# Kernel optimization log

Measured on AMD Instinct MI355X. Metric: run time of the kernel, lower is better.

Reference implementation:

```python
import jax, jax.numpy as jnp
import numpy as np

H_IMG = 224
W_IMG = 224
CHUNK = 128   # triangles rasterized per scan step
EPS = 1e-8
N_VERTS = 6890
N_FACES = 13776
BATCH = 2


def setup_inputs() -> dict:
    key = jax.random.key(0)
    k0, k1, k2 = jax.random.split(key, 3)
    # vertices in front of the camera (z ~ 2.5) so triangles project into the image
    v = jax.random.normal(k0, (BATCH, N_VERTS, 3), jnp.float32) * 0.3 + jnp.array([0.0, 0.0, 2.5], jnp.float32)
    vc = jax.random.uniform(k1, (N_VERTS, 3), dtype=jnp.float32)          # per-vertex colors
    f = jax.random.randint(k2, (N_FACES, 3), 0, N_VERTS, dtype=jnp.int32)  # triangle list
    bgcolor = jnp.zeros((3,), jnp.float32)
    camera_f = jnp.array([500.0, 500.0], jnp.float32)
    camera_c = jnp.array([112.0, 112.0], jnp.float32)
    camera_t = jnp.zeros((3,), jnp.float32)
    camera_rt = jnp.zeros((3,), jnp.float32)
    return {"v": v, "vc": vc, "bgcolor": bgcolor, "camera_f": camera_f,
            "camera_c": camera_c, "camera_t": camera_t, "camera_rt": camera_rt, "f": f}


def _rodrigues(r):
    # axis-angle -> rotation matrix, safe at r = 0
    th = jnp.sqrt(jnp.sum(r * r) + 1e-12)
    k = r / th
    kx, ky, kz = k[0], k[1], k[2]
    z = jnp.zeros_like(kx)
    K = jnp.stack([jnp.stack([z, -kz, ky]),
                   jnp.stack([kz, z, -kx]),
                   jnp.stack([-ky, kx, z])])
    c, s = jnp.cos(th), jnp.sin(th)
    return c * jnp.eye(3, dtype=r.dtype) + (1.0 - c) * jnp.outer(k, k) + s * K


def _edge(ax, ay, bx, by, px, py):
    # signed area of (a, b, p) * 2
    return (bx - ax) * (py - ay) - (by - ay) * (px - ax)


def _rasterize(uv, zc, vc, faces, bgcolor, height, width):
    """Z-buffered rasterization with perspective-correct barycentric color interp.
    uv: [V,2] screen coords, zc: [V] camera-space depth, vc: [V,C], faces: [F,3]."""
    F, C = faces.shape[0], vc.shape[-1]
    pad = (-F) % CHUNK
    faces_p = jnp.concatenate([faces, jnp.zeros((pad, 3), faces.dtype)], 0)
    fmask = jnp.concatenate([jnp.ones((F,), bool), jnp.zeros((pad,), bool)])
    faces_p = faces_p.reshape(-1, CHUNK, 3)
    fmask = fmask.reshape(-1, CHUNK)

    xs = jnp.arange(width, dtype=jnp.float32) + 0.5
    ys = jnp.arange(height, dtype=jnp.float32) + 0.5
    px, py = jnp.meshgrid(xs, ys)              # [H,W] pixel centers
    cx = px.ravel()[None, :]                    # [1,HW]
    cy = py.ravel()[None, :]
    HW = height * width
    ar = jnp.arange(HW)

    def step(carry, inp):
        zbuf, col = carry
        fc, fm = inp                            # [K,3] int, [K] bool
        p = uv[fc]                              # [K,3,2]
        zt = zc[fc]                             # [K,3]
        x0, y0 = p[:, 0, 0:1], p[:, 0, 1:2]
        x1, y1 = p[:, 1, 0:1], p[:, 1, 1:2]
        x2, y2 = p[:, 2, 0:1], p[:, 2, 1:2]
        w0 = _edge(x1, y1, x2, y2, cx, cy)      # [K,HW]
        w1 = _edge(x2, y2, x0, y0, cx, cy)
        w2 = _edge(x0, y0, x1, y1, cx, cy)
        area = _edge(x0, y0, x1, y1, x2, y2)    # [K,1]
        nz = jnp.abs(area) > EPS
        inv_area = jnp.where(nz, 1.0 / jnp.where(nz, area, 1.0), 0.0)
        b0, b1, b2 = w0 * inv_area, w1 * inv_area, w2 * inv_area
        inside = (b0 >= 0) & (b1 >= 0) & (b2 >= 0)
        zvalid = jnp.all(zt > EPS, axis=1, keepdims=True)
        valid = inside & zvalid & nz & fm[:, None]
        zt_s = jnp.maximum(zt, EPS)
        inv_z = b0 / zt_s[:, 0:1] + b1 / zt_s[:, 1:2] + b2 / zt_s[:, 2:3]
        zp = jnp.where(valid & (inv_z > EPS), 1.0 / jnp.maximum(inv_z, EPS), jnp.inf)
        idx = jnp.argmin(zp, axis=0)            # nearest triangle per pixel in chunk
        zmin = zp[idx, ar]                      # [HW]
        hit = jnp.isfinite(zmin)
        zmin_s = jnp.where(hit, zmin, 1.0)
        bb = jnp.stack([b0, b1, b2], -1)[idx, ar]   # [HW,3]
        fsel = fc[idx]                          # [HW,3]
        zsel = jnp.maximum(zt[idx], EPS)        # [HW,3]
        csel = vc[fsel]                         # [HW,3,C]
        pc = bb / zsel                          # perspective-correct weights / z
        newcol = jnp.einsum('pk,pkc->pc', pc, csel) * zmin_s[:, None]
        upd = hit & (zmin < zbuf)
        zbuf = jnp.where(upd, zmin_s, zbuf)
        col = jnp.where(upd[:, None], newcol, col)
        return (zbuf, col), None

    zbuf0 = jnp.full((HW,), jnp.inf, jnp.float32)
    col0 = jnp.broadcast_to(bgcolor.astype(jnp.float32), (HW, C))
    (zbuf, col), _ = jax.lax.scan(step, (zbuf0, col0), (faces_p, fmask))
    return col.reshape(height, width, C)


def reference(v, vc, bgcolor, camera_f, camera_c, camera_t, camera_rt, f):
    R = _rodrigues(camera_rt)
    vcam = jnp.einsum('bvj,ij->bvi', v, R) + camera_t   # [B,V,3]
    z = vcam[..., 2]
    zs = jnp.maximum(z, EPS)
    uv = vcam[..., :2] / zs[..., None] * camera_f + camera_c  # pinhole projection
    render = jax.vmap(lambda uv_b, z_b: _rasterize(uv_b, z_b, vc, f, bgcolor, H_IMG, W_IMG))
    return render(uv, z)                                   # [B,H,W,C]
```

## Files before the change

kernel.cpp:

```cpp
#include <hip/hip_runtime.h>
#include <math.h>

#define H_IMG 224
#define W_IMG 224
#define HW (H_IMG * W_IMG)
#define EPSF 1e-8f
#define NV 6890
#define NF 13776
#define NB 2
#define FCHUNK 128
#define NCHUNK ((NF + FCHUNK - 1) / FCHUNK)
#define FPAD (NCHUNK * FCHUNK)
#define NBUCK 1024
#define CHDR_STRIDE 128
#define KEY_INIT 0x7F800000FFFFFFFFULL

#define OFF_VERTS 0u
#define OFF_ZBU   220672u
#define OFF_ZBS   331008u
#define OFF_BBS   441600u
#define OFF_GMS   883968u
#define OFF_OIS   2653440u
#define OFF_INV   2764032u
#define OFF_CHDR  2874368u
#define OFF_CNT   2875392u
#define OFF_OFFS  2883584u

__device__ inline unsigned long long shfl_xor_u64(unsigned long long v, int m) {
  unsigned lo = (unsigned)v, hi = (unsigned)(v >> 32);
  lo = __shfl_xor(lo, m);
  hi = __shfl_xor(hi, m);
  return ((unsigned long long)hi << 32) | lo;
}

__global__ void proj_init_kernel(const float* __restrict__ v,
                                 const float* __restrict__ cf,
                                 const float* __restrict__ cc,
                                 const float* __restrict__ ct,
                                 const float* __restrict__ crt,
                                 float4* __restrict__ verts,
                                 float* __restrict__ zbS, float4* __restrict__ bbS,
                                 unsigned* __restrict__ chdr, unsigned* __restrict__ cnt) {
  int i = blockIdx.x * blockDim.x + threadIdx.x;
  if (i < NB * NV) {
    float r0 = crt[0], r1 = crt[1], r2 = crt[2];
    float ss = __fadd_rn(__fadd_rn(__fmul_rn(r0, r0), __fmul_rn(r1, r1)), __fmul_rn(r2, r2));
    float th = sqrtf(__fadd_rn(ss, 1e-12f));
    float kx = r0 / th, ky = r1 / th, kz = r2 / th;
    float c = cosf(th), s = sinf(th), oc = 1.0f - c;
    float R00 = c + oc * kx * kx,      R01 = oc * kx * ky - s * kz, R02 = oc * kx * kz + s * ky;
    float R10 = oc * ky * kx + s * kz, R11 = c + oc * ky * ky,      R12 = oc * ky * kz - s * kx;
    float R20 = oc * kz * kx - s * ky, R21 = oc * kz * ky + s * kx, R22 = c + oc * kz * kz;
    float x = v[i * 3 + 0], y = v[i * 3 + 1], z = v[i * 3 + 2];
    float xc = R00 * x + R01 * y + R02 * z + ct[0];
    float yc = R10 * x + R11 * y + R12 * z + ct[1];
    float zc = R20 * x + R21 * y + R22 * z + ct[2];
    float zs = fmaxf(zc, EPSF);
    float u = __fadd_rn(__fmul_rn(xc / zs, cf[0]), cc[0]);
    float w = __fadd_rn(__fmul_rn(yc / zs, cf[1]), cc[1]);
    verts[i] = make_float4(u, w, zc, 0.0f);
  }
  if (i < NB * FPAD) {
    zbS[i] = 3e30f;
    bbS[i] = make_float4(1e30f, -1e30f, 1e30f, -1e30f);
  }
  if (i < NB * CHDR_STRIDE) chdr[i] = 0x7F800000u;
  if (i < NB * NBUCK) cnt[i] = 0u;
}

__global__ void zb_kernel(const int* __restrict__ f, const float4* __restrict__ verts,
                          float* __restrict__ zbU, unsigned* __restrict__ cnt) {
  int i = blockIdx.x * blockDim.x + threadIdx.x;
  if (i >= NB * NF) return;
  int b = i / NF, fi = i - b * NF;
  int i0 = f[fi * 3 + 0], i1 = f[fi * 3 + 1], i2 = f[fi * 3 + 2];
  float4 p0 = verts[b * NV + i0], p1 = verts[b * NV + i1], p2 = verts[b * NV + i2];
  float area = __fsub_rn(__fmul_rn(__fsub_rn(p1.x, p0.x), __fsub_rn(p2.y, p0.y)),
                         __fmul_rn(__fsub_rn(p1.y, p0.y), __fsub_rn(p2.x, p0.x)));
  bool nz = fabsf(area) > EPSF;
  bool zv = (p0.z > EPSF) && (p1.z > EPSF) && (p2.z > EPSF);
  bool ok = nz && zv;
  float zb;
  if (!ok) {
    zb = 3e30f;
  } else {
    float minz = fminf(fminf(fmaxf(p0.z, EPSF), fmaxf(p1.z, EPSF)), fmaxf(p2.z, EPSF));
    float M = fmaxf(fmaxf(fmaxf(fabsf(p0.x), fabsf(p0.y)), fmaxf(fabsf(p1.x), fabsf(p1.y))),
                    fmaxf(fabsf(p2.x), fabsf(p2.y)));
    float werr = (2.0f * M) * (M + 256.0f) * 6e-7f;
    bool tight = (3.0f * werr) <= (5e-4f * fabsf(area));
    zb = tight ? __fmul_rn(minz, 0.999f) : 0.0f;
  }
  zbU[i] = zb;
  int bucket = (int)fminf(fmaxf(zb * 256.0f, 0.0f), (float)(NBUCK - 1));
  atomicAdd(&cnt[b * NBUCK + bucket], 1u);
}

__global__ __launch_bounds__(1024) void scan_kernel(const unsigned* __restrict__ cnt,
                                                    unsigned* __restrict__ offs) {
  __shared__ unsigned wsum[16];
  int t = threadIdx.x, b = blockIdx.x;
  int lane = t & 63, wid = t >> 6;
  unsigned v = cnt[b * NBUCK + t];
  unsigned acc = v;
  #pragma unroll
  for (int d = 1; d < 64; d <<= 1) {
    unsigned n = __shfl_up(acc, d);
    if (lane >= d) acc += n;
  }
  if (lane == 63) wsum[wid] = acc;
  __syncthreads();
  if (t < 16) {
    unsigned wv = wsum[t];
    #pragma unroll
    for (int d = 1; d < 16; d <<= 1) {
      unsigned n = __shfl_up(wv, d, 16);
      if (t >= d) wv += n;
    }
    wsum[t] = wv;
  }
  __syncthreads();
  unsigned base = (wid > 0) ? wsum[wid - 1] : 0u;
  offs[b * NBUCK + t] = base + acc - v;
}

__global__ void scatter_kernel(const int* __restrict__ f, const float4* __restrict__ verts,
                               const float* __restrict__ zbU, unsigned* __restrict__ offs,
                               float* __restrict__ zbS, float4* __restrict__ bbS,
                               float4* __restrict__ gmS, int* __restrict__ oiS,
                               int* __restrict__ inv, unsigned* __restrict__ chdr) {
  int i = blockIdx.x * blockDim.x + threadIdx.x;
  if (i >= NB * NF) return;
  int b = i / NF, fi = i - b * NF;
  float zb = zbU[i];
  int bucket = (int)fminf(fmaxf(zb * 256.0f, 0.0f), (float)(NBUCK - 1));
  unsigned pos = atomicAdd(&offs[b * NBUCK + bucket], 1u);
  int i0 = f[fi * 3 + 0], i1 = f[fi * 3 + 1], i2 = f[fi * 3 + 2];
  float4 p0 = verts[b * NV + i0], p1 = verts[b * NV + i1], p2 = verts[b * NV + i2];
  float x0 = p0.x, y0 = p0.y, z0 = p0.z;
  float x1 = p1.x, y1 = p1.y, z1 = p1.z;
  float x2 = p2.x, y2 = p2.y, z2 = p2.z;
  float area = __fsub_rn(__fmul_rn(__fsub_rn(x1, x0), __fsub_rn(y2, y0)),
                         __fmul_rn(__fsub_rn(y1, y0), __fsub_rn(x2, x0)));
  bool nz = fabsf(area) > EPSF;
  float inv_area = nz ? (1.0f / area) : 0.0f;
  bool zv = (z0 > EPSF) && (z1 > EPSF) && (z2 > EPSF);
  bool ok = nz && zv;
  float zz0 = ok ? fmaxf(z0, EPSF) : 1e30f;
  float zz1 = ok ? fmaxf(z1, EPSF) : 1e30f;
  float zz2 = ok ? fmaxf(z2, EPSF) : 1e30f;
  size_t sp_ = (size_t)b * FPAD + pos;
  zbS[sp_] = zb;
  bbS[sp_] = make_float4(fminf(fminf(x0, x1), x2), fmaxf(fmaxf(x0, x1), x2),
                         fminf(fminf(y0, y1), y2), fmaxf(fmaxf(y0, y1), y2));
  gmS[sp_ * 4 + 0] = make_float4(__fsub_rn(x2, x1), __fsub_rn(y2, y1), x1, y1);
  gmS[sp_ * 4 + 1] = make_float4(__fsub_rn(x0, x2), __fsub_rn(y0, y2), x2, y2);
  gmS[sp_ * 4 + 2] = make_float4(__fsub_rn(x1, x0), __fsub_rn(y1, y0), x0, y0);
  gmS[sp_ * 4 + 3] = make_float4(zz0, zz1, zz2, inv_area);
  oiS[sp_] = fi;
  inv[i] = (int)pos;
  atomicMin(&chdr[b * CHDR_STRIDE + (int)(pos / FCHUNK)], __float_as_uint(zb));
}

__global__ __launch_bounds__(CHDR_STRIDE) void suffix_kernel(unsigned* __restrict__ chdr) {
  __shared__ unsigned s[CHDR_STRIDE];
  int t = threadIdx.x, b = blockIdx.x;
  s[t] = chdr[b * CHDR_STRIDE + t];
  __syncthreads();
  for (int d = 1; d < CHDR_STRIDE; d <<= 1) {
    unsigned v = (t + d < CHDR_STRIDE) ? s[t + d] : 0x7F800000u;
    __syncthreads();
    s[t] = (v < s[t]) ? v : s[t];
    __syncthreads();
  }
  chdr[b * CHDR_STRIDE + t] = s[t];
}

__global__ __launch_bounds__(256) void raster_kernel(
    const unsigned* __restrict__ chdr,
    const float* __restrict__ zbS,
    const float4* __restrict__ bbS,
    const float4* __restrict__ gmS,
    const int* __restrict__ oiS,
    const int* __restrict__ inv,
    const int* __restrict__ f,
    const float* __restrict__ vc,
    const float* __restrict__ bg,
    float* __restrict__ out) {
  __shared__ unsigned hint[4][16];
  __shared__ unsigned long long fin[4][16];
  int b = blockIdx.z;
  int w = threadIdx.x >> 6;
  int lane = threadIdx.x & 63;
  int slot = lane & 3;
  int p = lane >> 2;
  int wx = blockIdx.x * 4, wy = blockIdx.y * 4;
  int x = wx + (p & 3), y = wy + (p >> 2);
  float px = (float)x + 0.5f, py = (float)y + 0.5f;
  float tx0 = (float)wx + 0.5f, tx1 = (float)wx + 3.5f;
  float ty0 = (float)wy + 0.5f, ty1 = (float)wy + 3.5f;
  const unsigned* chdrB = chdr + b * CHDR_STRIDE;
  const float*  zbB = zbS + (size_t)b * FPAD;
  const float4* bbB = bbS + (size_t)b * FPAD;
  const float4* gmB = gmS + (size_t)b * FPAD * 4;
  const int*    oiB = oiS + (size_t)b * FPAD;

  if (threadIdx.x < 64) hint[threadIdx.x >> 4][threadIdx.x & 15] = 0x7F800000u;
  __syncthreads();

  unsigned long long bestKey = KEY_INIT;

  for (int c = w; c < NCHUNK; c += 4) {
    unsigned z_ = (unsigned)(bestKey >> 32);
    unsigned zo = __shfl_xor(z_, 1); if (zo < z_) z_ = zo;
    zo = __shfl_xor(z_, 2); if (zo < z_) z_ = zo;
    if (slot == 0) hint[w][p] = z_;
    unsigned bzp = hint[0][p];
    unsigned h1 = hint[1][p]; if (h1 < bzp) bzp = h1;
    unsigned h2 = hint[2][p]; if (h2 < bzp) bzp = h2;
    unsigned h3 = hint[3][p]; if (h3 < bzp) bzp = h3;
    float comb = __uint_as_float(bzp);
    float czb = __uint_as_float(chdrB[c]);
    if (!__any(czb <= comb)) break;
    float combMax = fmaxf(comb, __shfl_xor(comb, 4));
    combMax = fmaxf(combMax, __shfl_xor(combMax, 8));
    combMax = fmaxf(combMax, __shfl_xor(combMax, 16));
    combMax = fmaxf(combMax, __shfl_xor(combMax, 32));
    int base = c * FCHUNK;
    #pragma unroll
    for (int h = 0; h < FCHUNK / 64; ++h) {
      int fbase = base + h * 64;
      float zb_lane = zbB[fbase + lane];
      float4 bb = bbB[fbase + lane];
      bool pass = (zb_lane <= combMax) &&
                  (bb.x <= tx1) && (bb.y >= tx0) &&
                  (bb.z <= ty1) && (bb.w >= ty0);
      unsigned long long m = __ballot(pass);
      unsigned long long mm = m;
      while (mm) {
        int bit = __builtin_ctzll(mm);
        int g = bit & ~3;
        mm &= ~(0xFULL << g);
        if ((m >> (g + slot)) & 1) {
          int fi = fbase + g + slot;
          const float4* gm = &gmB[(size_t)fi * 4];
          float4 q0 = gm[0], q1 = gm[1], q2 = gm[2], q3 = gm[3];
          float w0 = __fsub_rn(__fmul_rn(q0.x, __fsub_rn(py, q0.w)),
                               __fmul_rn(q0.y, __fsub_rn(px, q0.z)));
          float w1 = __fsub_rn(__fmul_rn(q1.x, __fsub_rn(py, q1.w)),
                               __fmul_rn(q1.y, __fsub_rn(px, q1.z)));
          float w2 = __fsub_rn(__fmul_rn(q2.x, __fsub_rn(py, q2.w)),
                               __fmul_rn(q2.y, __fsub_rn(px, q2.z)));
          float b0 = __fmul_rn(w0, q3.w);
          float b1 = __fmul_rn(w1, q3.w);
          float b2 = __fmul_rn(w2, q3.w);
          if (b0 >= 0.0f && b1 >= 0.0f && b2 >= 0.0f) {
            float invz = __fadd_rn(__fadd_rn(b0 / q3.x, b1 / q3.y), b2 / q3.z);
            if (invz > EPSF) {
              float zp = 1.0f / invz;
              unsigned long long key =
                  ((unsigned long long)__float_as_uint(zp) << 32) | (unsigned)oiB[fi];
              if (key < bestKey) bestKey = key;
            }
          }
        }
      }
    }
  }

  unsigned long long o = shfl_xor_u64(bestKey, 1);
  if (o < bestKey) bestKey = o;
  o = shfl_xor_u64(bestKey, 2);
  if (o < bestKey) bestKey = o;
  if (slot == 0) fin[w][p] = bestKey;
  __syncthreads();

  int t = threadIdx.x;
  if (t < 16) {
    unsigned long long key = fin[0][t];
    unsigned long long k1 = fin[1][t]; if (k1 < key) key = k1;
    unsigned long long k2 = fin[2][t]; if (k2 < key) key = k2;
    unsigned long long k3 = fin[3][t]; if (k3 < key) key = k3;
    int xx = wx + (t & 3), yy = wy + (t >> 2);
    float pxx = (float)xx + 0.5f, pyy = (float)yy + 0.5f;
    float o0, o1, o2;
    if (key != KEY_INIT) {
      int best = (int)(unsigned)(key & 0xFFFFFFFFu);
      float zmin = __uint_as_float((unsigned)(key >> 32));
      int pos = inv[b * NF + best];
      const float4* g = &gmB[(size_t)pos * 4];
      float4 q0 = g[0], q1 = g[1], q2 = g[2], q3 = g[3];
      float w0 = __fsub_rn(__fmul_rn(q0.x, __fsub_rn(pyy, q0.w)),
                           __fmul_rn(q0.y, __fsub_rn(pxx, q0.z)));
      float w1 = __fsub_rn(__fmul_rn(q1.x, __fsub_rn(pyy, q1.w)),
                           __fmul_rn(q1.y, __fsub_rn(pxx, q1.z)));
      float w2 = __fsub_rn(__fmul_rn(q2.x, __fsub_rn(pyy, q2.w)),
                           __fmul_rn(q2.y, __fsub_rn(pxx, q2.z)));
      float b0 = __fmul_rn(w0, q3.w), b1 = __fmul_rn(w1, q3.w), b2 = __fmul_rn(w2, q3.w);
      float pc0 = b0 / q3.x, pc1 = b1 / q3.y, pc2 = b2 / q3.z;
      int i0 = f[best * 3 + 0], i1 = f[best * 3 + 1], i2 = f[best * 3 + 2];
      const float* c0p = vc + (size_t)i0 * 3;
      const float* c1p = vc + (size_t)i1 * 3;
      const float* c2p = vc + (size_t)i2 * 3;
      o0 = __fmul_rn(__fadd_rn(__fadd_rn(__fmul_rn(pc0, c0p[0]), __fmul_rn(pc1, c1p[0])),
                               __fmul_rn(pc2, c2p[0])), zmin);
      o1 = __fmul_rn(__fadd_rn(__fadd_rn(__fmul_rn(pc0, c0p[1]), __fmul_rn(pc1, c1p[1])),
                               __fmul_rn(pc2, c2p[1])), zmin);
      o2 = __fmul_rn(__fadd_rn(__fadd_rn(__fmul_rn(pc0, c0p[2]), __fmul_rn(pc1, c1p[2])),
                               __fmul_rn(pc2, c2p[2])), zmin);
    } else {
      o0 = bg[0]; o1 = bg[1]; o2 = bg[2];
    }
    size_t oo = ((size_t)(b * H_IMG + yy) * W_IMG + xx) * 3;
    out[oo + 0] = o0;
    out[oo + 1] = o1;
    out[oo + 2] = o2;
  }
}

extern "C" void kernel_launch(void* const* d_in, const int* in_sizes, int n_in,
                              void* d_out, int out_size, void* d_ws, size_t ws_size,
                              hipStream_t stream) {
  const float* v   = (const float*)d_in[0];
  const float* vc  = (const float*)d_in[1];
  const float* bg  = (const float*)d_in[2];
  const float* cf  = (const float*)d_in[3];
  const float* cc  = (const float*)d_in[4];
  const float* ct  = (const float*)d_in[5];
  const float* crt = (const float*)d_in[6];
  const int*   f   = (const int*)d_in[7];
  float* out = (float*)d_out;
  char* ws = (char*)d_ws;

  float4*   verts = (float4*)(ws + OFF_VERTS);
  float*    zbU   = (float*)(ws + OFF_ZBU);
  float*    zbS   = (float*)(ws + OFF_ZBS);
  float4*   bbS   = (float4*)(ws + OFF_BBS);
  float4*   gmS   = (float4*)(ws + OFF_GMS);
  int*      oiS   = (int*)(ws + OFF_OIS);
  int*      inv   = (int*)(ws + OFF_INV);
  unsigned* chdr  = (unsigned*)(ws + OFF_CHDR);
  unsigned* cnt   = (unsigned*)(ws + OFF_CNT);
  unsigned* offs  = (unsigned*)(ws + OFF_OFFS);

  hipLaunchKernelGGL(proj_init_kernel, dim3((NB * HW + 255) / 256), dim3(256), 0, stream,
                     v, cf, cc, ct, crt, verts, zbS, bbS, chdr, cnt);
  hipLaunchKernelGGL(zb_kernel, dim3((NB * NF + 255) / 256), dim3(256), 0, stream,
                     f, verts, zbU, cnt);
  hipLaunchKernelGGL(scan_kernel, dim3(NB), dim3(1024), 0, stream, cnt, offs);
  hipLaunchKernelGGL(scatter_kernel, dim3((NB * NF + 255) / 256), dim3(256), 0, stream,
                     f, verts, zbU, offs, zbS, bbS, gmS, oiS, inv, chdr);
  hipLaunchKernelGGL(suffix_kernel, dim3(NB), dim3(CHDR_STRIDE), 0, stream, chdr);
  hipLaunchKernelGGL(raster_kernel, dim3(W_IMG / 4, H_IMG / 4, NB),
                     dim3(256), 0, stream,
                     chdr, zbS, bbS, gmS, oiS, inv, f, vc, bg, out);
}
```

Baseline: 302.1 us.

## Fuse projection into face kernels, derive chunk bounds in scan, use 8 waves

Removes the separate vertex-projection kernel: each face kernel now recomputes the camera transform and projects its three vertices inline. The per-chunk minimum-depth header is computed in the scan kernel by binary search over bucket ends, which drops the atomicMin in scatter and the suffix kernel. The count reset moves to a memset, and the raster kernel grows from 4 to 8 waves per tile to split the chunk loop further. This trades fewer launches and atomics for redundant projection math, a coarser bucket-level depth bound, and more waves contending on the shared hint.

```diff
diff --git a/kernel.cpp b/kernel.cpp
--- a/kernel.cpp
+++ b/kernel.cpp
@@ -11,20 +11,20 @@
 #define FCHUNK 128
 #define NCHUNK ((NF + FCHUNK - 1) / FCHUNK)
 #define FPAD (NCHUNK * FCHUNK)
+#define NWAVE 8
 #define NBUCK 1024
 #define CHDR_STRIDE 128
 #define KEY_INIT 0x7F800000FFFFFFFFULL
 
-#define OFF_VERTS 0u
-#define OFF_ZBU   220672u
-#define OFF_ZBS   331008u
-#define OFF_BBS   441600u
-#define OFF_GMS   883968u
-#define OFF_OIS   2653440u
-#define OFF_INV   2764032u
-#define OFF_CHDR  2874368u
-#define OFF_CNT   2875392u
-#define OFF_OFFS  2883584u
+#define OFF_ZBU   0u
+#define OFF_ZBS   110336u
+#define OFF_BBS   220928u
+#define OFF_GMS   663296u
+#define OFF_OIS   2432768u
+#define OFF_INV   2543360u
+#define OFF_CHDR  2653696u
+#define OFF_CNT   2654720u
+#define OFF_OFFS  2662912u
 
 __device__ inline unsigned long long shfl_xor_u64(unsigned long long v, int m) {
   unsigned lo = (unsigned)v, hi = (unsigned)(v >> 32);
@@ -33,48 +33,52 @@
   return ((unsigned long long)hi << 32) | lo;
 }
 
-__global__ void proj_init_kernel(const float* __restrict__ v,
-                                 const float* __restrict__ cf,
-                                 const float* __restrict__ cc,
-                                 const float* __restrict__ ct,
-                                 const float* __restrict__ crt,
-                                 float4* __restrict__ verts,
-                                 float* __restrict__ zbS, float4* __restrict__ bbS,
-                                 unsigned* __restrict__ chdr, unsigned* __restrict__ cnt) {
+struct Cam { float m[9]; float t0, t1, t2, fx, fy, cx, cy; };
+
+__device__ inline Cam load_cam(const float* cf, const float* cc,
+                               const float* ct, const float* crt) {
+  Cam C;
+  float r0 = crt[0], r1 = crt[1], r2 = crt[2];
+  float ss = __fadd_rn(__fadd_rn(__fmul_rn(r0, r0), __fmul_rn(r1, r1)), __fmul_rn(r2, r2));
+  float th = sqrtf(__fadd_rn(ss, 1e-12f));
+  float kx = r0 / th, ky = r1 / th, kz = r2 / th;
+  float c = cosf(th), s = sinf(th), oc = 1.0f - c;
+  C.m[0] = c + oc * kx * kx;      C.m[1] = oc * kx * ky - s * kz; C.m[2] = oc * kx * kz + s * ky;
+  C.m[3] = oc * ky * kx + s * kz; C.m[4] = c + oc * ky * ky;      C.m[5] = oc * ky * kz - s * kx;
+  C.m[6] = oc * kz * kx - s * ky; C.m[7] = oc * kz * ky + s * kx; C.m[8] = c + oc * kz * kz;
+  C.t0 = ct[0]; C.t1 = ct[1]; C.t2 = ct[2];
+  C.fx = cf[0]; C.fy = cf[1]; C.cx = cc[0]; C.cy = cc[1];
+  return C;
+}
+
+__device__ inline float3 proj_one(const Cam& C, const float* vp) {
+  float x = vp[0], y = vp[1], z = vp[2];
+  float xc = C.m[0] * x + C.m[1] * y + C.m[2] * z + C.t0;
+  float yc = C.m[3] * x + C.m[4] * y + C.m[5] * z + C.t1;
+  float zc = C.m[6] * x + C.m[7] * y + C.m[8] * z + C.t2;
+  float zs = fmaxf(zc, EPSF);
+  float u = __fadd_rn(__fmul_rn(xc / zs, C.fx), C.cx);
+  float w = __fadd_rn(__fmul_rn(yc / zs, C.fy), C.cy);
+  return make_float3(u, w, zc);
+}
+
+__global__ void zb_init_kernel(const float* __restrict__ v, const int* __restrict__ f,
+                               const float* __restrict__ cf, const float* __restrict__ cc,
+                               const float* __restrict__ ct, const float* __restrict__ crt,
+                               float* __restrict__ zbU, unsigned* __restrict__ cnt,
+                               float* __restrict__ zbS, float4* __restrict__ bbS) {
   int i = blockIdx.x * blockDim.x + threadIdx.x;
-  if (i < NB * NV) {
-    float r0 = crt[0], r1 = crt[1], r2 = crt[2];
-    float ss = __fadd_rn(__fadd_rn(__fmul_rn(r0, r0), __fmul_rn(r1, r1)), __fmul_rn(r2, r2));
-    float th = sqrtf(__fadd_rn(ss, 1e-12f));
-    float kx = r0 / th, ky = r1 / th, kz = r2 / th;
-    float c = cosf(th), s = sinf(th), oc = 1.0f - c;
-    float R00 = c + oc * kx * kx,      R01 = oc * kx * ky - s * kz, R02 = oc * kx * kz + s * ky;
-    float R10 = oc * ky * kx + s * kz, R11 = c + oc * ky * ky,      R12 = oc * ky * kz - s * kx;
-    float R20 = oc * kz * kx - s * ky, R21 = oc * kz * ky + s * kx, R22 = c + oc * kz * kz;
-    float x = v[i * 3 + 0], y = v[i * 3 + 1], z = v[i * 3 + 2];
-    float xc = R00 * x + R01 * y + R02 * z + ct[0];
-    float yc = R10 * x + R11 * y + R12 * z + ct[1];
-    float zc = R20 * x + R21 * y + R22 * z + ct[2];
-    float zs = fmaxf(zc, EPSF);
-    float u = __fadd_rn(__fmul_rn(xc / zs, cf[0]), cc[0]);
-    float w = __fadd_rn(__fmul_rn(yc / zs, cf[1]), cc[1]);
-    verts[i] = make_float4(u, w, zc, 0.0f);
-  }
   if (i < NB * FPAD) {
     zbS[i] = 3e30f;
     bbS[i] = make_float4(1e30f, -1e30f, 1e30f, -1e30f);
   }
-  if (i < NB * CHDR_STRIDE) chdr[i] = 0x7F800000u;
-  if (i < NB * NBUCK) cnt[i] = 0u;
-}
-
-__global__ void zb_kernel(const int* __restrict__ f, const float4* __restrict__ verts,
-                          float* __restrict__ zbU, unsigned* __restrict__ cnt) {
-  int i = blockIdx.x * blockDim.x + threadIdx.x;
   if (i >= NB * NF) return;
   int b = i / NF, fi = i - b * NF;
+  Cam C = load_cam(cf, cc, ct, crt);
   int i0 = f[fi * 3 + 0], i1 = f[fi * 3 + 1], i2 = f[fi * 3 + 2];
-  float4 p0 = verts[b * NV + i0], p1 = verts[b * NV + i1], p2 = verts[b * NV + i2];
+  float3 p0 = proj_one(C, v + ((size_t)b * NV + i0) * 3);
+  float3 p1 = proj_one(C, v + ((size_t)b * NV + i1) * 3);
+  float3 p2 = proj_one(C, v + ((size_t)b * NV + i2) * 3);
   float area = __fsub_rn(__fmul_rn(__fsub_rn(p1.x, p0.x), __fsub_rn(p2.y, p0.y)),
                          __fmul_rn(__fsub_rn(p1.y, p0.y), __fsub_rn(p2.x, p0.x)));
   bool nz = fabsf(area) > EPSF;
@@ -97,8 +101,10 @@
 }
 
 __global__ __launch_bounds__(1024) void scan_kernel(const unsigned* __restrict__ cnt,
-                                                    unsigned* __restrict__ offs) {
+                                                    unsigned* __restrict__ offs,
+                                                    unsigned* __restrict__ chdr) {
   __shared__ unsigned wsum[16];
+  __shared__ unsigned ends[NBUCK];
   int t = threadIdx.x, b = blockIdx.x;
   int lane = t & 63, wid = t >> 6;
   unsigned v = cnt[b * NBUCK + t];
@@ -121,22 +127,39 @@
   }
   __syncthreads();
   unsigned base = (wid > 0) ? wsum[wid - 1] : 0u;
-  offs[b * NBUCK + t] = base + acc - v;
-}
-
-__global__ void scatter_kernel(const int* __restrict__ f, const float4* __restrict__ verts,
+  unsigned incl = base + acc;
+  offs[b * NBUCK + t] = incl - v;
+  ends[t] = incl;
+  __syncthreads();
+  if (t < NCHUNK) {
+    unsigned pos0 = (unsigned)(t * FCHUNK);
+    int lo = 0, hi = NBUCK - 1;
+    while (lo < hi) {
+      int mid = (lo + hi) >> 1;
+      if (ends[mid] > pos0) hi = mid; else lo = mid + 1;
+    }
+    chdr[b * CHDR_STRIDE + t] = __float_as_uint((float)lo * (1.0f / 256.0f));
+  }
+}
+
+__global__ void scatter_kernel(const float* __restrict__ v, const int* __restrict__ f,
+                               const float* __restrict__ cf, const float* __restrict__ cc,
+                               const float* __restrict__ ct, const float* __restrict__ crt,
                                const float* __restrict__ zbU, unsigned* __restrict__ offs,
                                float* __restrict__ zbS, float4* __restrict__ bbS,
                                float4* __restrict__ gmS, int* __restrict__ oiS,
-                               int* __restrict__ inv, unsigned* __restrict__ chdr) {
+                               int* __restrict__ inv) {
   int i = blockIdx.x * blockDim.x + threadIdx.x;
   if (i >= NB * NF) return;
   int b = i / NF, fi = i - b * NF;
   float zb = zbU[i];
   int bucket = (int)fminf(fmaxf(zb * 256.0f, 0.0f), (float)(NBUCK - 1));
   unsigned pos = atomicAdd(&offs[b * NBUCK + bucket], 1u);
+  Cam C = load_cam(cf, cc, ct, crt);
   int i0 = f[fi * 3 + 0], i1 = f[fi * 3 + 1], i2 = f[fi * 3 + 2];
-  float4 p0 = verts[b * NV + i0], p1 = verts[b * NV + i1], p2 = verts[b * NV + i2];
+  float3 p0 = proj_one(C, v + ((size_t)b * NV + i0) * 3);
+  float3 p1 = proj_one(C, v + ((size_t)b * NV + i1) * 3);
+  float3 p2 = proj_one(C, v + ((size_t)b * NV + i2) * 3);
   float x0 = p0.x, y0 = p0.y, z0 = p0.z;
   float x1 = p1.x, y1 = p1.y, z1 = p1.z;
   float x2 = p2.x, y2 = p2.y, z2 = p2.z;
@@ -159,24 +182,9 @@
   gmS[sp_ * 4 + 3] = make_float4(zz0, zz1, zz2, inv_area);
   oiS[sp_] = fi;
   inv[i] = (int)pos;
-  atomicMin(&chdr[b * CHDR_STRIDE + (int)(pos / FCHUNK)], __float_as_uint(zb));
-}
-
-__global__ __launch_bounds__(CHDR_STRIDE) void suffix_kernel(unsigned* __restrict__ chdr) {
-  __shared__ unsigned s[CHDR_STRIDE];
-  int t = threadIdx.x, b = blockIdx.x;
-  s[t] = chdr[b * CHDR_STRIDE + t];
-  __syncthreads();
-  for (int d = 1; d < CHDR_STRIDE; d <<= 1) {
-    unsigned v = (t + d < CHDR_STRIDE) ? s[t + d] : 0x7F800000u;
-    __syncthreads();
-    s[t] = (v < s[t]) ? v : s[t];
-    __syncthreads();
-  }
-  chdr[b * CHDR_STRIDE + t] = s[t];
-}
-
-__global__ __launch_bounds__(256) void raster_kernel(
+}
+
+__global__ __launch_bounds__(512) void raster_kernel(
     const unsigned* __restrict__ chdr,
     const float* __restrict__ zbS,
     const float4* __restrict__ bbS,
@@ -187,8 +195,8 @@
     const float* __restrict__ vc,
     const float* __restrict__ bg,
     float* __restrict__ out) {
-  __shared__ unsigned hint[4][16];
-  __shared__ unsigned long long fin[4][16];
+  __shared__ unsigned hint[NWAVE][16];
+  __shared__ unsigned long long fin[NWAVE][16];
   int b = blockIdx.z;
   int w = threadIdx.x >> 6;
   int lane = threadIdx.x & 63;
@@ -205,20 +213,21 @@
   const float4* gmB = gmS + (size_t)b * FPAD * 4;
   const int*    oiB = oiS + (size_t)b * FPAD;
 
-  if (threadIdx.x < 64) hint[threadIdx.x >> 4][threadIdx.x & 15] = 0x7F800000u;
+  if (threadIdx.x < NWAVE * 16) hint[threadIdx.x >> 4][threadIdx.x & 15] = 0x7F800000u;
   __syncthreads();
 
   unsigned long long bestKey = KEY_INIT;
 
-  for (int c = w; c < NCHUNK; c += 4) {
+  for (int c = w; c < NCHUNK; c += NWAVE) {
     unsigned z_ = (unsigned)(bestKey >> 32);
     unsigned zo = __shfl_xor(z_, 1); if (zo < z_) z_ = zo;
     zo = __shfl_xor(z_, 2); if (zo < z_) z_ = zo;
     if (slot == 0) hint[w][p] = z_;
     unsigned bzp = hint[0][p];
-    unsigned h1 = hint[1][p]; if (h1 < bzp) bzp = h1;
-    unsigned h2 = hint[2][p]; if (h2 < bzp) bzp = h2;
-    unsigned h3 = hint[3][p]; if (h3 < bzp) bzp = h3;
+    #pragma unroll
+    for (int hw_ = 1; hw_ < NWAVE; ++hw_) {
+      unsigned hh = hint[hw_][p]; if (hh < bzp) bzp = hh;
+    }
     float comb = __uint_as_float(bzp);
     float czb = __uint_as_float(chdrB[c]);
     if (!__any(czb <= comb)) break;
@@ -278,9 +287,10 @@
   int t = threadIdx.x;
   if (t < 16) {
     unsigned long long key = fin[0][t];
-    unsigned long long k1 = fin[1][t]; if (k1 < key) key = k1;
-    unsigned long long k2 = fin[2][t]; if (k2 < key) key = k2;
-    unsigned long long k3 = fin[3][t]; if (k3 < key) key = k3;
+    #pragma unroll
+    for (int hw_ = 1; hw_ < NWAVE; ++hw_) {
+      unsigned long long kk = fin[hw_][t]; if (kk < key) key = kk;
+    }
     int xx = wx + (t & 3), yy = wy + (t >> 2);
     float pxx = (float)xx + 0.5f, pyy = (float)yy + 0.5f;
     float o0, o1, o2;
@@ -332,7 +342,6 @@
   float* out = (float*)d_out;
   char* ws = (char*)d_ws;
 
-  float4*   verts = (float4*)(ws + OFF_VERTS);
   float*    zbU   = (float*)(ws + OFF_ZBU);
   float*    zbS   = (float*)(ws + OFF_ZBS);
   float4*   bbS   = (float4*)(ws + OFF_BBS);
@@ -343,15 +352,13 @@
   unsigned* cnt   = (unsigned*)(ws + OFF_CNT);
   unsigned* offs  = (unsigned*)(ws + OFF_OFFS);
 
-  hipLaunchKernelGGL(proj_init_kernel, dim3((NB * HW + 255) / 256), dim3(256), 0, stream,
-                     v, cf, cc, ct, crt, verts, zbS, bbS, chdr, cnt);
-  hipLaunchKernelGGL(zb_kernel, dim3((NB * NF + 255) / 256), dim3(256), 0, stream,
-                     f, verts, zbU, cnt);
-  hipLaunchKernelGGL(scan_kernel, dim3(NB), dim3(1024), 0, stream, cnt, offs);
+  hipMemsetAsync(cnt, 0, (size_t)NB * NBUCK * 4, stream);
+  hipLaunchKernelGGL(zb_init_kernel, dim3((NB * FPAD + 255) / 256), dim3(256), 0, stream,
+                     v, f, cf, cc, ct, crt, zbU, cnt, zbS, bbS);
+  hipLaunchKernelGGL(scan_kernel, dim3(NB), dim3(1024), 0, stream, cnt, offs, chdr);
   hipLaunchKernelGGL(scatter_kernel, dim3((NB * NF + 255) / 256), dim3(256), 0, stream,
-                     f, verts, zbU, offs, zbS, bbS, gmS, oiS, inv, chdr);
-  hipLaunchKernelGGL(suffix_kernel, dim3(NB), dim3(CHDR_STRIDE), 0, stream, chdr);
+                     v, f, cf, cc, ct, crt, zbU, offs, zbS, bbS, gmS, oiS, inv);
   hipLaunchKernelGGL(raster_kernel, dim3(W_IMG / 4, H_IMG / 4, NB),
-                     dim3(256), 0, stream,
+                     dim3(512), 0, stream,
                      chdr, zbS, bbS, gmS, oiS, inv, f, vc, bg, out);
 }
```

Measured after the change: 339.2 us. 1.12x slower.
